# Optimization experiments

Measured on AMD Instinct MI355X. Metric: run time of the kernel, lower is better.

The kernel has to match this reference:

```python
import jax, jax.numpy as jnp
import numpy as np

N_NODES = 50000
N_EDGES = 800000
D = 128          # input_dim == output_dim
H = 2 * D        # hidden size = 2*output_dim
EPS = 1e-5       # BatchNorm1d eps


def _mlp(x, W1, b1, g1, beta1, W2, b2):
    # Linear -> BatchNorm1d (training-mode batch stats) -> ReLU -> Linear
    y = x @ W1 + b1
    mu = jnp.mean(y, axis=0)
    var = jnp.mean(jnp.square(y - mu), axis=0)  # biased var, as used for normalization
    y = (y - mu) * jax.lax.rsqrt(var + EPS) * g1 + beta1
    y = jax.nn.relu(y)
    return y @ W2 + b2


def setup_inputs() -> dict:
    key = jax.random.key(0)
    ks = jax.random.split(key, 16)
    h = jax.random.normal(ks[0], (N_NODES, D), dtype=jnp.float32)
    e = jax.random.normal(ks[1], (N_EDGES, D), dtype=jnp.float32)
    src = jax.random.randint(ks[2], (N_EDGES,), 0, N_NODES, dtype=jnp.int32)
    dst = jax.random.randint(ks[3], (N_EDGES,), 0, N_NODES, dtype=jnp.int32)

    def lin(k, fan_in, fan_out):
        return jax.random.normal(k, (fan_in, fan_out), dtype=jnp.float32) * (1.0 / np.sqrt(fan_in))

    params = {
        # mlp_bond: in 2D -> H -> D
        'W1b': lin(ks[4], 2 * D, H), 'b1b': jnp.zeros((H,), jnp.float32),
        'g1b': jnp.ones((H,), jnp.float32), 'beta1b': jnp.zeros((H,), jnp.float32),
        'W2b': lin(ks[5], H, D), 'b2b': jnp.zeros((D,), jnp.float32),
        # mlp_atom: in 2D -> H -> D
        'W1a': lin(ks[6], 2 * D, H), 'b1a': jnp.zeros((H,), jnp.float32),
        'g1a': jnp.ones((H,), jnp.float32), 'beta1a': jnp.zeros((H,), jnp.float32),
        'W2a': lin(ks[7], H, D), 'b2a': jnp.zeros((D,), jnp.float32),
    }
    return {'h': h, 'e': e, 'src': src, 'dst': dst, **params}


def reference(h, e, src, dst,
              W1b, b1b, g1b, beta1b, W2b, b2b,
              W1a, b1a, g1a, beta1a, W2a, b2a):
    # --- bond update: gather u_add_v, concat with e, MLP ---
    sum_h_edge = h[src] + h[dst]                              # [E, D]
    e_new = _mlp(jnp.concatenate([sum_h_edge, e], axis=-1),
                 W1b, b1b, g1b, beta1b, W2b, b2b)             # [E, D]

    # --- atom update: scatter-sum of src node feats and NEW edge feats to dst ---
    sum_h = jax.ops.segment_sum(h[src], dst, num_segments=N_NODES)   # copy_u + sum
    sum_e = jax.ops.segment_sum(e_new, dst, num_segments=N_NODES)   # copy_e + sum
    h_new = _mlp(jnp.concatenate([sum_h, sum_e], axis=-1),
                 W1a, b1a, g1a, beta1a, W2a, b2a)             # [N, D]

    # out_batch_norm=False, out_activation=None, residual=False, dropout=None
    return h_new, e_new
```

## Files before the change

### kernel.cpp

```cpp
#include <hip/hip_runtime.h>
#include <hip/hip_bf16.h>
#include <stdint.h>

#define DD 128
#define HH 256
#define EPSBN 1e-5f

typedef __attribute__((ext_vector_type(4))) float f32x4;
typedef __attribute__((ext_vector_type(8))) short s16x8;
typedef __attribute__((ext_vector_type(4))) short s16x4;

__device__ __forceinline__ unsigned short f2bf(float f){
  union { __hip_bfloat16 h; unsigned short u; } v;
  v.h = __float2bfloat16(f);
  return v.u;
}
__device__ __forceinline__ float bf2f(unsigned short s){
  union{unsigned u; float f;} v; v.u=((unsigned)s)<<16; return v.f;
}
__device__ __forceinline__ int swz(int row, int kb){ return row*512 + (kb ^ ((row&31)<<4)); }

__global__ void wt_kernel(const float* __restrict__ W1b, const float* __restrict__ W2b,
                          const float* __restrict__ W1a, const float* __restrict__ W2a,
                          unsigned short* __restrict__ WT1b, unsigned short* __restrict__ WT2b,
                          unsigned short* __restrict__ WT1a, unsigned short* __restrict__ WT2a){
  int idx = blockIdx.x*256 + threadIdx.x;
  if (idx < 65536){ int n=idx>>8, k=idx&255; WT1b[n*256+k]=f2bf(W1b[k*256+n]); }
  else if (idx < 98304){ int t=idx-65536; int n=t>>8, k=t&255; WT2b[n*256+k]=f2bf(W2b[k*128+n]); }
  else if (idx < 163840){ int t=idx-98304; int n=t>>8, k=t&255; WT1a[n*256+k]=f2bf(W1a[k*256+n]); }
  else if (idx < 196608){ int t=idx-163840; int n=t>>8, k=t&255; WT2a[n*256+k]=f2bf(W2a[k*128+n]); }
}

__global__ void h2bf_hist_kernel(const float* __restrict__ h, unsigned short* __restrict__ hb, int n8,
                                 const int* __restrict__ dst, int* __restrict__ counts, int E){
  int i = blockIdx.x*256 + threadIdx.x;
  if (i < n8){
    f32x4 a = *(const f32x4*)(h + (size_t)i*8);
    f32x4 b = *(const f32x4*)(h + (size_t)i*8 + 4);
    s16x8 p;
    #pragma unroll
    for (int q=0;q<4;q++){ p[q]=(short)f2bf(a[q]); p[4+q]=(short)f2bf(b[q]); }
    *(s16x8*)(hb + (size_t)i*8) = p;
  }
  if (i < E) atomicAdd(&counts[dst[i]], 1);
}

__global__ void scan_kernel(const int* __restrict__ counts, int* __restrict__ offsets,
                            int* __restrict__ cursor, int n){
  __shared__ int wsum[16];
  int tid = threadIdx.x, lane = tid&63, wid = tid>>6;
  int carry = 0;
  int nch = (n + 1023)/1024;
  for (int ch=0; ch<nch; ch++){
    int i = ch*1024 + tid;
    int v = (i<n)? counts[i] : 0;
    int s = v;
    #pragma unroll
    for (int off=1; off<64; off<<=1){ int t = __shfl_up(s, off); if (lane>=off) s += t; }
    if (lane==63) wsum[wid] = s;
    __syncthreads();
    int woff = 0, tot = 0;
    #pragma unroll
    for (int w=0; w<16; w++){ int t = wsum[w]; if (w<wid) woff += t; tot += t; }
    if (i<n){ int excl = carry + woff + s - v; offsets[i]=excl; cursor[i]=excl; }
    carry += tot;
    __syncthreads();
  }
  if (tid==0) offsets[n] = carry;
}

__global__ void fill_kernel(const int* __restrict__ dst, const int* __restrict__ srcv,
                            int* __restrict__ cursor,
                            int* __restrict__ eids, int* __restrict__ esrc, int E){
  int i = blockIdx.x*256 + threadIdx.x;
  if (i < E){
    int slot = atomicAdd(&cursor[dst[i]], 1);
    eids[slot] = i;
    esrc[slot] = srcv[i];
  }
}

__device__ __forceinline__ void gemm1_core(char* xt, const s16x8 (&Bf)[8][2],
                                           float bias0, float bias1,
                                           unsigned short* __restrict__ yout,
                                           float* __restrict__ stats,
                                           int base, int nrows)
{
  const int tid = threadIdx.x;
  const int l = tid&63, w = tid>>6, lr = l&15, lg = l>>4;
  const int nb = w*32;
  f32x4 acc[4][2];
  #pragma unroll
  for (int mt=0;mt<4;mt++)
    #pragma unroll
    for (int nt=0;nt<2;nt++) acc[mt][nt] = (f32x4){0.f,0.f,0.f,0.f};
  #pragma unroll
  for (int kc=0;kc<8;kc++){
    s16x8 af[4];
    #pragma unroll
    for (int mt=0;mt<4;mt++)
      af[mt] = *(const s16x8*)(xt + swz(mt*16 + lr, kc*64 + lg*16));
    #pragma unroll
    for (int nt=0;nt<2;nt++)
      #pragma unroll
      for (int mt=0;mt<4;mt++)
        acc[mt][nt] = __builtin_amdgcn_mfma_f32_16x16x32_bf16(af[mt], Bf[kc][nt], acc[mt][nt], 0,0,0);
  }
  float st1a=0.f, st1b=0.f, st2a=0.f, st2b=0.f;
  #pragma unroll
  for (int mt=0;mt<4;mt++)
    #pragma unroll
    for (int q=0;q<4;q++){
      float m = (base + mt*16 + lg*4 + q < nrows) ? 1.0f : 0.0f;
      float v0 = (acc[mt][0][q] + bias0)*m;
      float v1 = (acc[mt][1][q] + bias1)*m;
      st1a += v0; st2a += v0*v0;
      st1b += v1; st2b += v1*v1;
    }
  __syncthreads();
  #pragma unroll
  for (int mt=0;mt<4;mt++)
    #pragma unroll
    for (int q=0;q<4;q++){
      *(unsigned short*)(xt + (mt*16 + lg*4 + q)*512 + (nb + lr)*2)      = f2bf(acc[mt][0][q] + bias0);
      *(unsigned short*)(xt + (mt*16 + lg*4 + q)*512 + (nb + 16 + lr)*2) = f2bf(acc[mt][1][q] + bias1);
    }
  __syncthreads();
  #pragma unroll
  for (int it=0;it<4;it++){
    int off = it*8192 + tid*16;
    int row = off >> 9;
    if (base + row < nrows)
      *(s16x8*)((char*)yout + (size_t)base*512 + off) = *(const s16x8*)(xt + off);
  }
  {
    int rep = blockIdx.x & 63;
    float s;
    s = st1a; s += __shfl_xor(s,16); s += __shfl_xor(s,32);
    if (l < 16) atomicAdd(&stats[rep*512 + nb + lr], s);
    s = st2a; s += __shfl_xor(s,16); s += __shfl_xor(s,32);
    if (l < 16) atomicAdd(&stats[rep*512 + 256 + nb + lr], s);
    s = st1b; s += __shfl_xor(s,16); s += __shfl_xor(s,32);
    if (l < 16) atomicAdd(&stats[rep*512 + nb + 16 + lr], s);
    s = st2b; s += __shfl_xor(s,16); s += __shfl_xor(s,32);
    if (l < 16) atomicAdd(&stats[rep*512 + 256 + nb + 16 + lr], s);
  }
}

__global__ __launch_bounds__(512, 4) void edge_mlp1(
    const unsigned short* __restrict__ hb, const float* __restrict__ e,
    const int* __restrict__ src, const int* __restrict__ dstv,
    const unsigned short* __restrict__ WT1, const float* __restrict__ b1,
    unsigned short* __restrict__ yout, float* __restrict__ stats, int E)
{
  __shared__ alignas(16) char xt[32768];
  const int tid = threadIdx.x;
  const int l = tid&63, w = tid>>6, lr = l&15, lg = l>>4;
  const int nb = w*32;
  const int base = blockIdx.x*64;

  const int r = tid>>3, jj = tid&7;
  const int ei = base + r;
  int s_ = src[ei], d_ = dstv[ei];

  const int cb = tid&31, r0 = tid>>5;
  f32x4 ev[4];
  #pragma unroll
  for (int k=0;k<4;k++)
    ev[k] = *(const f32x4*)(e + (size_t)(base + r0 + k*16)*DD + cb*4);

  const s16x8* hs = (const s16x8*)(hb + (size_t)s_*DD) + jj*2;
  const s16x8* hd = (const s16x8*)(hb + (size_t)d_*DD) + jj*2;
  s16x8 a0=hs[0], a1=hs[1], c0=hd[0], c1=hd[1];

  #pragma unroll
  for (int k=0;k<4;k++){
    s16x4 p;
    #pragma unroll
    for (int q=0;q<4;q++) p[q] = (short)f2bf(ev[k][q]);
    *(s16x4*)(xt + swz(r0 + k*16, 256 + cb*8)) = p;
  }
  {
    s16x8 o0, o1;
    #pragma unroll
    for (int q=0;q<8;q++){
      o0[q] = (short)f2bf(bf2f((unsigned short)a0[q]) + bf2f((unsigned short)c0[q]));
      o1[q] = (short)f2bf(bf2f((unsigned short)a1[q]) + bf2f((unsigned short)c1[q]));
    }
    *(s16x8*)(xt + swz(r, jj*32))      = o0;
    *(s16x8*)(xt + swz(r, jj*32 + 16)) = o1;
  }
  s16x8 Bf[8][2];
  #pragma unroll
  for (int kc=0;kc<8;kc++)
    #pragma unroll
    for (int nt=0;nt<2;nt++)
      Bf[kc][nt] = *(const s16x8*)(WT1 + (size_t)(nb + nt*16 + lr)*256 + kc*32 + lg*8);
  float bias0 = b1[nb+lr], bias1 = b1[nb+16+lr];
  __syncthreads();
  gemm1_core(xt, Bf, bias0, bias1, yout, stats, base, E);
}

__global__ __launch_bounds__(512, 4) void node_mlp1(
    const unsigned short* __restrict__ hb, const float* __restrict__ enew,
    const int* __restrict__ offsets, const int* __restrict__ eids, const int* __restrict__ esrc,
    const unsigned short* __restrict__ WT1, const float* __restrict__ b1,
    unsigned short* __restrict__ yout, float* __restrict__ stats, int NN)
{
  __shared__ alignas(16) char xt[32768];
  const int tid = threadIdx.x;
  const int l = tid&63, w = tid>>6, lr = l&15, lg = l>>4;
  const int nb = w*32;
  const int base = blockIdx.x*64;
  const int r = tid>>3, jj = tid&7;
  const int node = base + r;

  float ah[16], ae[16];
  #pragma unroll
  for (int q=0;q<16;q++){ ah[q]=0.f; ae[q]=0.f; }
  if (node < NN){
    int beg = offsets[node], end = offsets[node+1];
    if (beg < end){
      int eid = eids[beg];
      int s_  = esrc[beg];
      for (int p = beg; p < end; p++){
        int pn = (p+1 < end) ? p+1 : p;
        int eid_n = eids[pn];
        int s_n   = esrc[pn];
        const s16x8* hsp = (const s16x8*)(hb + (size_t)s_*DD + jj*16);
        const f32x4* ep = (const f32x4*)(enew + (size_t)eid*DD + jj*16);
        s16x8 a0 = hsp[0], a1 = hsp[1];
        f32x4 e0 = ep[0], e1 = ep[1], e2 = ep[2], e3 = ep[3];
        #pragma unroll
        for (int q=0;q<8;q++){ ah[q] += bf2f((unsigned short)a0[q]); ah[8+q] += bf2f((unsigned short)a1[q]); }
        #pragma unroll
        for (int q=0;q<4;q++){ ae[q] += e0[q]; ae[4+q] += e1[q]; ae[8+q] += e2[q]; ae[12+q] += e3[q]; }
        eid = eid_n; s_ = s_n;
      }
    }
  }
  {
    s16x8 o0, o1;
    #pragma unroll
    for (int q=0;q<8;q++){ o0[q] = (short)f2bf(ah[q]); o1[q] = (short)f2bf(ah[8+q]); }
    *(s16x8*)(xt + swz(r, jj*32))      = o0;
    *(s16x8*)(xt + swz(r, jj*32 + 16)) = o1;
    #pragma unroll
    for (int q=0;q<8;q++){ o0[q] = (short)f2bf(ae[q]); o1[q] = (short)f2bf(ae[8+q]); }
    *(s16x8*)(xt + swz(r, 256 + jj*32))      = o0;
    *(s16x8*)(xt + swz(r, 256 + jj*32 + 16)) = o1;
  }
  s16x8 Bf[8][2];
  #pragma unroll
  for (int kc=0;kc<8;kc++)
    #pragma unroll
    for (int nt=0;nt<2;nt++)
      Bf[kc][nt] = *(const s16x8*)(WT1 + (size_t)(nb + nt*16 + lr)*256 + kc*32 + lg*8);
  float bias0 = b1[nb+lr], bias1 = b1[nb+16+lr];
  __syncthreads();
  gemm1_core(xt, Bf, bias0, bias1, yout, stats, base, NN);
}

__global__ void finalize_kernel(const float* __restrict__ stats, const float* __restrict__ g,
                                const float* __restrict__ beta, float* __restrict__ scale, float invcnt){
  __shared__ float red[512];
  int tid = threadIdx.x;
  float s = 0.f;
  for (int rep=0; rep<64; rep++) s += stats[rep*512 + tid];
  red[tid] = s;
  __syncthreads();
  if (tid < 256){
    float mu  = red[tid]*invcnt;
    float var = red[256+tid]*invcnt - mu*mu;
    float a = g[tid] * rsqrtf(var + EPSBN);
    float c = beta[tid] - mu*a;
    scale[2*tid] = a; scale[2*tid+1] = c;
  }
}

__global__ __launch_bounds__(512, 4) void mlp2_kernel(const unsigned short* y,
    const unsigned short* __restrict__ WT2, const float* __restrict__ b2,
    const float* __restrict__ scale, float* outp, int nrows)
{
  __shared__ alignas(16) char xt[32768];
  const int tid = threadIdx.x;
  const int l = tid&63, w = tid>>6, lr = l&15, lg = l>>4;
  const int nb = w*16;
  const int base0 = blockIdx.x*128;

  s16x8 Bf[8];
  #pragma unroll
  for (int kc=0;kc<8;kc++)
    Bf[kc] = *(const s16x8*)(WT2 + (size_t)(nb + lr)*HH + kc*32 + lg*8);
  float bias = b2[nb+lr];
  const int cb = tid&31, r0 = tid>>5;
  float sa[8], sc[8];
  #pragma unroll
  for (int q=0;q<8;q++){ sa[q]=scale[2*(cb*8+q)]; sc[q]=scale[2*(cb*8+q)+1]; }

  #pragma unroll 1
  for (int t=0;t<2;t++){
    const int base = base0 + t*64;
    #pragma unroll
    for (int k=0;k<4;k++){
      int r = r0 + k*16;
      s16x8 raw = {0,0,0,0,0,0,0,0};
      if (base + r < nrows) raw = *(const s16x8*)(y + (size_t)(base+r)*HH + cb*8);
      s16x8 o;
      #pragma unroll
      for (int q=0;q<8;q++){
        float f = fmaxf(bf2f((unsigned short)raw[q])*sa[q] + sc[q], 0.0f);
        o[q] = (short)f2bf(f);
      }
      *(s16x8*)(xt + swz(r, cb*16)) = o;
    }
    __syncthreads();
    f32x4 acc[4];
    #pragma unroll
    for (int mt=0;mt<4;mt++) acc[mt] = (f32x4){0.f,0.f,0.f,0.f};
    #pragma unroll
    for (int kc=0;kc<8;kc++){
      s16x8 af[4];
      #pragma unroll
      for (int mt=0;mt<4;mt++)
        af[mt] = *(const s16x8*)(xt + swz(mt*16 + lr, kc*64 + lg*16));
      #pragma unroll
      for (int mt=0;mt<4;mt++)
        acc[mt] = __builtin_amdgcn_mfma_f32_16x16x32_bf16(af[mt], Bf[kc], acc[mt], 0,0,0);
    }
    __syncthreads();
    #pragma unroll
    for (int mt=0;mt<4;mt++)
      #pragma unroll
      for (int q=0;q<4;q++)
        *(float*)(xt + (mt*16 + lg*4 + q)*512 + (nb + lr)*4) = acc[mt][q] + bias;
    __syncthreads();
    #pragma unroll
    for (int it=0;it<4;it++){
      int off = it*8192 + tid*16;
      int row = off >> 9;
      if (base + row < nrows)
        *(f32x4*)(outp + (size_t)(base+row)*DD + ((off&511)>>2)) = *(const f32x4*)(xt + off);
    }
    if (t==0) __syncthreads();
  }
}

extern "C" void kernel_launch(void* const* d_in, const int* in_sizes, int n_in,
                              void* d_out, int out_size, void* d_ws, size_t ws_size,
                              hipStream_t stream) {
  const float* h    = (const float*)d_in[0];
  const float* e    = (const float*)d_in[1];
  const int*   src  = (const int*)d_in[2];
  const int*   dst  = (const int*)d_in[3];
  const float* W1b  = (const float*)d_in[4];
  const float* b1b  = (const float*)d_in[5];
  const float* g1b  = (const float*)d_in[6];
  const float* beta1b=(const float*)d_in[7];
  const float* W2b  = (const float*)d_in[8];
  const float* b2b  = (const float*)d_in[9];
  const float* W1a  = (const float*)d_in[10];
  const float* b1a  = (const float*)d_in[11];
  const float* g1a  = (const float*)d_in[12];
  const float* beta1a=(const float*)d_in[13];
  const float* W2a  = (const float*)d_in[14];
  const float* b2a  = (const float*)d_in[15];

  const int E  = in_sizes[2];
  const int NN = in_sizes[0] / DD;

  char* ws = (char*)d_ws;
  unsigned short* WT1b = (unsigned short*)(ws + 0);
  unsigned short* WT2b = (unsigned short*)(ws + 131072);
  unsigned short* WT1a = (unsigned short*)(ws + 196608);
  unsigned short* WT2a = (unsigned short*)(ws + 327680);
  float* scaleE = (float*)(ws + 393216);
  float* scaleN = (float*)(ws + 395264);
  float* statsE = (float*)(ws + 397312);
  float* statsN = (float*)(ws + 528384);
  int* counts  = (int*)(ws + 659456);
  int* offsets = (int*)(ws + 860160);
  int* cursor  = (int*)(ws + 1060864);
  int* eids    = (int*)(ws + 1261568);
  unsigned short* ya = (unsigned short*)(ws + 4461568);
  unsigned short* hb = (unsigned short*)(ws + 30086144);
  int* esrc   = (int*)(ws + 42886144);

  float* outH = (float*)d_out;
  float* outE = outH + (size_t)NN * DD;
  unsigned short* yE = (unsigned short*)outE;

  hipMemsetAsync(ws + 397312, 0, 131072 + 131072 + 200704, stream);

  wt_kernel<<<768, 256, 0, stream>>>(W1b, W2b, W1a, W2a, WT1b, WT2b, WT1a, WT2a);
  h2bf_hist_kernel<<<(NN*DD/8 + 255)/256, 256, 0, stream>>>(h, hb, NN*DD/8, dst, counts, E);
  scan_kernel<<<1, 1024, 0, stream>>>(counts, offsets, cursor, NN);
  fill_kernel<<<(E+255)/256, 256, 0, stream>>>(dst, src, cursor, eids, esrc, E);

  const int tE64  = E/64;
  const int tE128 = E/128;
  const int tN64  = (NN + 63)/64;
  const int tN128 = (NN + 127)/128;

  edge_mlp1<<<tE64, 512, 0, stream>>>(hb, e, src, dst, WT1b, b1b, yE, statsE, E);
  finalize_kernel<<<1, 512, 0, stream>>>(statsE, g1b, beta1b, scaleE, 1.0f/(float)E);
  mlp2_kernel<<<tE128, 512, 0, stream>>>(yE, WT2b, b2b, scaleE, outE, E);
  node_mlp1<<<tN64, 512, 0, stream>>>(hb, outE, offsets, eids, esrc, WT1a, b1a, ya, statsN, NN);
  finalize_kernel<<<1, 512, 0, stream>>>(statsN, g1a, beta1a, scaleN, 1.0f/(float)NN);
  mlp2_kernel<<<tN128, 512, 0, stream>>>(ya, WT2a, b2a, scaleN, outH, NN);
}
```

Baseline: 776.2 us.

## Stream weight fragments in halves to cut registers and raise occupancy

Instead of preloading all B-fragments of the weight matrix into registers before the GEMM, the weights are loaded in two halves inside the K loop, and bias loads are moved after the MFMA loop. Launch bounds are raised from 4 to 6 blocks per SM for the edge, node and mlp2 kernels to exploit the lower register pressure. This aims to hide the gather and memory latency better through occupancy, at the cost of re-reading weights (from L2/L1) per block half and less overlap between weight loads and the gather phase. LDS use of 32KB per block may cap the extra occupancy anyway.

```diff
diff --git a/kernel.cpp b/kernel.cpp
--- a/kernel.cpp
+++ b/kernel.cpp
@@ -80,8 +80,8 @@
   }
 }
 
-__device__ __forceinline__ void gemm1_core(char* xt, const s16x8 (&Bf)[8][2],
-                                           float bias0, float bias1,
+__device__ __forceinline__ void gemm1_core(char* xt, const unsigned short* __restrict__ WT,
+                                           const float* __restrict__ b1,
                                            unsigned short* __restrict__ yout,
                                            float* __restrict__ stats,
                                            int base, int nrows)
@@ -94,18 +94,26 @@
   for (int mt=0;mt<4;mt++)
     #pragma unroll
     for (int nt=0;nt<2;nt++) acc[mt][nt] = (f32x4){0.f,0.f,0.f,0.f};
-  #pragma unroll
-  for (int kc=0;kc<8;kc++){
-    s16x8 af[4];
-    #pragma unroll
-    for (int mt=0;mt<4;mt++)
-      af[mt] = *(const s16x8*)(xt + swz(mt*16 + lr, kc*64 + lg*16));
-    #pragma unroll
-    for (int nt=0;nt<2;nt++)
-      #pragma unroll
-      for (int mt=0;mt<4;mt++)
-        acc[mt][nt] = __builtin_amdgcn_mfma_f32_16x16x32_bf16(af[mt], Bf[kc][nt], acc[mt][nt], 0,0,0);
-  }
+  #pragma unroll 1
+  for (int hf=0; hf<2; hf++){
+    s16x8 Bf[4][2];
+    #pragma unroll
+    for (int k4=0;k4<4;k4++)
+      #pragma unroll
+      for (int nt=0;nt<2;nt++)
+        Bf[k4][nt] = *(const s16x8*)(WT + (size_t)(nb + nt*16 + lr)*256 + (hf*4+k4)*32 + lg*8);
+    #pragma unroll
+    for (int k4=0;k4<4;k4++){
+      const int kc = hf*4 + k4;
+      #pragma unroll
+      for (int mt=0;mt<4;mt++){
+        s16x8 af = *(const s16x8*)(xt + swz(mt*16 + lr, kc*64 + lg*16));
+        acc[mt][0] = __builtin_amdgcn_mfma_f32_16x16x32_bf16(af, Bf[k4][0], acc[mt][0], 0,0,0);
+        acc[mt][1] = __builtin_amdgcn_mfma_f32_16x16x32_bf16(af, Bf[k4][1], acc[mt][1], 0,0,0);
+      }
+    }
+  }
+  float bias0 = b1[nb+lr], bias1 = b1[nb+16+lr];
   float st1a=0.f, st1b=0.f, st2a=0.f, st2b=0.f;
   #pragma unroll
   for (int mt=0;mt<4;mt++)
@@ -147,7 +155,7 @@
   }
 }
 
-__global__ __launch_bounds__(512, 4) void edge_mlp1(
+__global__ __launch_bounds__(512, 6) void edge_mlp1(
     const unsigned short* __restrict__ hb, const float* __restrict__ e,
     const int* __restrict__ src, const int* __restrict__ dstv,
     const unsigned short* __restrict__ WT1, const float* __restrict__ b1,
@@ -155,8 +163,6 @@
 {
   __shared__ alignas(16) char xt[32768];
   const int tid = threadIdx.x;
-  const int l = tid&63, w = tid>>6, lr = l&15, lg = l>>4;
-  const int nb = w*32;
   const int base = blockIdx.x*64;
 
   const int r = tid>>3, jj = tid&7;
@@ -190,18 +196,11 @@
     *(s16x8*)(xt + swz(r, jj*32))      = o0;
     *(s16x8*)(xt + swz(r, jj*32 + 16)) = o1;
   }
-  s16x8 Bf[8][2];
-  #pragma unroll
-  for (int kc=0;kc<8;kc++)
-    #pragma unroll
-    for (int nt=0;nt<2;nt++)
-      Bf[kc][nt] = *(const s16x8*)(WT1 + (size_t)(nb + nt*16 + lr)*256 + kc*32 + lg*8);
-  float bias0 = b1[nb+lr], bias1 = b1[nb+16+lr];
   __syncthreads();
-  gemm1_core(xt, Bf, bias0, bias1, yout, stats, base, E);
-}
-
-__global__ __launch_bounds__(512, 4) void node_mlp1(
+  gemm1_core(xt, WT1, b1, yout, stats, base, E);
+}
+
+__global__ __launch_bounds__(512, 6) void node_mlp1(
     const unsigned short* __restrict__ hb, const float* __restrict__ enew,
     const int* __restrict__ offsets, const int* __restrict__ eids, const int* __restrict__ esrc,
     const unsigned short* __restrict__ WT1, const float* __restrict__ b1,
@@ -209,8 +208,6 @@
 {
   __shared__ alignas(16) char xt[32768];
   const int tid = threadIdx.x;
-  const int l = tid&63, w = tid>>6, lr = l&15, lg = l>>4;
-  const int nb = w*32;
   const int base = blockIdx.x*64;
   const int r = tid>>3, jj = tid&7;
   const int node = base + r;
@@ -250,15 +247,8 @@
     *(s16x8*)(xt + swz(r, 256 + jj*32))      = o0;
     *(s16x8*)(xt + swz(r, 256 + jj*32 + 16)) = o1;
   }
-  s16x8 Bf[8][2];
-  #pragma unroll
-  for (int kc=0;kc<8;kc++)
-    #pragma unroll
-    for (int nt=0;nt<2;nt++)
-      Bf[kc][nt] = *(const s16x8*)(WT1 + (size_t)(nb + nt*16 + lr)*256 + kc*32 + lg*8);
-  float bias0 = b1[nb+lr], bias1 = b1[nb+16+lr];
   __syncthreads();
-  gemm1_core(xt, Bf, bias0, bias1, yout, stats, base, NN);
+  gemm1_core(xt, WT1, b1, yout, stats, base, NN);
 }
 
 __global__ void finalize_kernel(const float* __restrict__ stats, const float* __restrict__ g,
@@ -278,7 +268,7 @@
   }
 }
 
-__global__ __launch_bounds__(512, 4) void mlp2_kernel(const unsigned short* y,
+__global__ __launch_bounds__(512, 6) void mlp2_kernel(const unsigned short* y,
     const unsigned short* __restrict__ WT2, const float* __restrict__ b2,
     const float* __restrict__ scale, float* outp, int nrows)
 {
@@ -288,11 +278,6 @@
   const int nb = w*16;
   const int base0 = blockIdx.x*128;
 
-  s16x8 Bf[8];
-  #pragma unroll
-  for (int kc=0;kc<8;kc++)
-    Bf[kc] = *(const s16x8*)(WT2 + (size_t)(nb + lr)*HH + kc*32 + lg*8);
-  float bias = b2[nb+lr];
   const int cb = tid&31, r0 = tid>>5;
   float sa[8], sc[8];
   #pragma unroll
@@ -318,16 +303,23 @@
     f32x4 acc[4];
     #pragma unroll
     for (int mt=0;mt<4;mt++) acc[mt] = (f32x4){0.f,0.f,0.f,0.f};
-    #pragma unroll
-    for (int kc=0;kc<8;kc++){
-      s16x8 af[4];
-      #pragma unroll
-      for (int mt=0;mt<4;mt++)
-        af[mt] = *(const s16x8*)(xt + swz(mt*16 + lr, kc*64 + lg*16));
-      #pragma unroll
-      for (int mt=0;mt<4;mt++)
-        acc[mt] = __builtin_amdgcn_mfma_f32_16x16x32_bf16(af[mt], Bf[kc], acc[mt], 0,0,0);
-    }
+    #pragma unroll 1
+    for (int hf=0; hf<2; hf++){
+      s16x8 Bf[4];
+      #pragma unroll
+      for (int k4=0;k4<4;k4++)
+        Bf[k4] = *(const s16x8*)(WT2 + (size_t)(nb + lr)*HH + (hf*4+k4)*32 + lg*8);
+      #pragma unroll
+      for (int k4=0;k4<4;k4++){
+        const int kc = hf*4 + k4;
+        #pragma unroll
+        for (int mt=0;mt<4;mt++){
+          s16x8 af = *(const s16x8*)(xt + swz(mt*16 + lr, kc*64 + lg*16));
+          acc[mt] = __builtin_amdgcn_mfma_f32_16x16x32_bf16(af, Bf[k4], acc[mt], 0,0,0);
+        }
+      }
+    }
+    float bias = b2[nb+lr];
     __syncthreads();
     #pragma unroll
     for (int mt=0;mt<4;mt++)
```

New measurement: 841.7 us. +8.4%, slower.
